# Kernel optimization log

Measured on AMD Instinct MI355X. Metric: run time of the kernel, lower is better.

Reference implementation:

```python
import jax, jax.numpy as jnp
import numpy as np

N, R, H0, H1, E, NB = 50000, 16, 128, 64, 800000, 8


def setup_inputs() -> dict:
    key = jax.random.key(0)
    k = jax.random.split(key, 6)
    nodes = jax.random.normal(k[0], (N, H0), dtype=jnp.float32)
    comps = jax.random.normal(k[1], (R, NB), dtype=jnp.float32) * 0.1
    bases = jax.random.normal(k[2], (NB, H0, H1), dtype=jnp.float32) * 0.05
    bias = jnp.zeros((H1,), dtype=jnp.float32)
    src = jax.random.randint(k[3], (E,), 0, N)
    rel = jax.random.randint(k[4], (E,), 0, R)
    dst = jax.random.randint(k[5], (E,), 0, N)
    return {"nodes": nodes, "comps": comps, "bases": bases, "bias": bias,
            "src": src, "rel": rel, "dst": dst}


def reference(nodes, comps, bases, bias, src, rel, dst):
    n, h0 = nodes.shape
    r = comps.shape[0]
    # Edge normalization: util.sum_sparse on the VERTICAL stacking -> row index
    # is rel*n + src, so each edge value is 1 / (#edges with same (rel, subject)).
    row = rel * n + src  # (E,)
    counts = jax.ops.segment_sum(jnp.ones(src.shape, jnp.float32), row, num_segments=r * n)
    vals = 1.0 / counts[row]  # (E,)
    # Basis decomposition: weights[r] = sum_b comps[r,b] * bases[b]
    weights = jnp.einsum('rb,bio->rio', comps, bases)  # (r, h0, h1)
    # Per-relation transformed node features (equivalent to expand + 'rni,rio->rno')
    nw = jnp.einsum('ni,rio->rno', nodes, weights)  # (r, n, h1)
    # Horizontal sparse mm: out[s] += val * nw[rel, dst]
    msgs = nw[rel, dst] * vals[:, None]  # (E, h1) gather
    out = jax.ops.segment_sum(msgs, src, num_segments=n)  # (n, h1) scatter-add
    return out + bias
```

## Files before the change

kernel.cpp:

```cpp
#include <hip/hip_runtime.h>
#include <hip/hip_bf16.h>

#define NN 50000
#define RR 16
#define H0 128
#define H1 64
#define EE 800000
#define NBASE 8
#define NTILES (NN / 16)
#define NGRPS ((NTILES + 3) / 4)
#define GEMM_BLOCKS NGRPS
#define COUNT_BLOCKS ((EE + 255) / 256)
#define NM (NN * RR)
#define NB1 782

typedef __attribute__((ext_vector_type(8))) short short8;
typedef __attribute__((ext_vector_type(4))) short short4v;
typedef __attribute__((ext_vector_type(4))) float f32x4;

__device__ inline short f2bs(float x) {
    __hip_bfloat16 b = __float2bfloat16(x);
    return *reinterpret_cast<short*>(&b);
}

__global__ void k_prep(const float* __restrict__ comps, const float* __restrict__ bases,
                       __hip_bfloat16* __restrict__ wtT, int* __restrict__ cnt) {
    if (blockIdx.x < 512) {
        int idx = blockIdx.x * 256 + threadIdx.x;
        int r = idx / (H1 * H0);
        int rem = idx % (H1 * H0);
        int o = rem / H0;
        int i = rem % H0;
        float acc = 0.0f;
#pragma unroll
        for (int b = 0; b < NBASE; ++b)
            acc += comps[r * NBASE + b] * bases[(b * H0 + i) * H1 + o];
        wtT[idx] = __float2bfloat16(acc);
    } else {
        int g = (blockIdx.x - 512) * 256 + threadIdx.x;
        if (g * 4 < NM) *(int4*)&cnt[g * 4] = (int4){0, 0, 0, 0};
    }
}

__global__ __launch_bounds__(256, 1)
void k_fused(const float* __restrict__ nodes,
             const __hip_bfloat16* __restrict__ wtT,
             __hip_bfloat16* __restrict__ nw,
             const int* __restrict__ src, const int* __restrict__ rel,
             int* __restrict__ cnt, int* __restrict__ rank) {
    __shared__ __hip_bfloat16 asmem[64 * 128];
    if (blockIdx.x < GEMM_BLOCKS) {
        int tid  = threadIdx.x;
        int ngrp = blockIdx.x;
        int ntl = NTILES - ngrp * 4;
        if (ntl > 4) ntl = 4;

#pragma unroll
        for (int i = 0; i < 8; ++i) {
            int f = i * 256 + tid;
            int row = f >> 5;
            int chunk = f & 31;
            int node = ngrp * 64 + row;
            if (node > NN - 1) node = NN - 1;
            float4 v = *(const float4*)&nodes[(size_t)node * H0 + chunk * 4];
            short4v o;
            o[0] = f2bs(v.x); o[1] = f2bs(v.y); o[2] = f2bs(v.z); o[3] = f2bs(v.w);
            int blk = chunk >> 1, half = chunk & 1;
            *(short4v*)((char*)asmem + row * 256 + ((blk ^ (row & 7)) << 4) + half * 8) = o;
        }
        __syncthreads();

        int wid  = tid >> 6;
        int lane = tid & 63;
        int rg   = wid;
        int n16  = lane & 15;
        int kg   = lane >> 4;

        short8 afrag[4][4];
#pragma unroll
        for (int t = 0; t < 4; ++t) {
            if (t < ntl) {
                int r = t * 16 + n16;
#pragma unroll
                for (int ks = 0; ks < 4; ++ks)
                    afrag[t][ks] = *(const short8*)((char*)asmem + r * 256 +
                                                    (((ks * 4 + kg) ^ (n16 & 7)) << 4));
            }
        }

        int chb = (n16 >> 2) * 16 + (n16 & 3);

        for (int r0 = 0; r0 < 4; ++r0) {
            int r = rg * 4 + r0;
            const __hip_bfloat16* wrr = &wtT[((size_t)r * H1 + chb) * H0 + kg * 8];
            f32x4 acc[4][4];
#pragma unroll
            for (int ot = 0; ot < 4; ++ot)
#pragma unroll
                for (int t = 0; t < 4; ++t) acc[ot][t] = (f32x4){0, 0, 0, 0};

#pragma unroll
            for (int ot = 0; ot < 4; ++ot) {
#pragma unroll
                for (int ks = 0; ks < 4; ++ks) {
                    short8 w = *(const short8*)(wrr + (size_t)(ot * 4) * H0 + ks * 32);
                    acc[ot][0] = __builtin_amdgcn_mfma_f32_16x16x32_bf16(w, afrag[0][ks], acc[ot][0], 0, 0, 0);
                    acc[ot][1] = __builtin_amdgcn_mfma_f32_16x16x32_bf16(w, afrag[1][ks], acc[ot][1], 0, 0, 0);
                    acc[ot][2] = __builtin_amdgcn_mfma_f32_16x16x32_bf16(w, afrag[2][ks], acc[ot][2], 0, 0, 0);
                    acc[ot][3] = __builtin_amdgcn_mfma_f32_16x16x32_bf16(w, afrag[3][ks], acc[ot][3], 0, 0, 0);
                }
            }

#pragma unroll
            for (int t = 0; t < 4; ++t) {
                if (t >= ntl) break;
                unsigned pk[8];
#pragma unroll
                for (int j = 0; j < 8; ++j) {
                    f32x4 a = acc[j >> 1][t];
                    float lo = a[(j & 1) * 2], hi = a[(j & 1) * 2 + 1];
                    pk[j] = (unsigned)(unsigned short)f2bs(lo) |
                            ((unsigned)(unsigned short)f2bs(hi) << 16);
                }
                uint4 q0; q0.x = pk[0]; q0.y = pk[1]; q0.z = pk[2]; q0.w = pk[3];
                uint4 q1; q1.x = pk[4]; q1.y = pk[5]; q1.z = pk[6]; q1.w = pk[7];
                char* rowp = (char*)nw +
                             ((size_t)r * NN + (size_t)ngrp * 64 + t * 16 + n16) * 128;
                *(uint4*)(rowp + kg * 16)      = q0;
                *(uint4*)(rowp + 64 + kg * 16) = q1;
            }
        }
    } else {
        int e = (blockIdx.x - GEMM_BLOCKS) * 256 + threadIdx.x;
        if (e < EE) {
            int bin = src[e] * RR + rel[e];
            rank[e] = atomicAdd(&cnt[bin], 1);
        }
    }
}

__global__ void k_scan1(const int* __restrict__ cnt, int* __restrict__ base2,
                        int* __restrict__ bsums) {
    __shared__ int tmp[256];
    int tid = threadIdx.x;
    int g = blockIdx.x * 256 + tid;
    int4 v = {0, 0, 0, 0};
    if (g * 4 < NM) v = *(const int4*)&cnt[g * 4];
    int s = v.x + v.y + v.z + v.w;
    tmp[tid] = s;
    __syncthreads();
    for (int off = 1; off < 256; off <<= 1) {
        int t = (tid >= off) ? tmp[tid - off] : 0;
        __syncthreads();
        tmp[tid] += t;
        __syncthreads();
    }
    int excl = tmp[tid] - s;
    if (tid == 255) bsums[blockIdx.x] = tmp[255];
    if (g * 4 < NM) {
        int4 o;
        o.x = excl;
        o.y = excl + v.x;
        o.z = excl + v.x + v.y;
        o.w = excl + v.x + v.y + v.z;
        *(int4*)&base2[g * 4] = o;
    }
}

__global__ void k_scan2(const int* __restrict__ bsums, int* __restrict__ bsofs) {
    __shared__ int tmp[256];
    int t = threadIdx.x;
    int i0 = t * 4;
    int v0 = (i0 < NB1) ? bsums[i0] : 0;
    int v1 = (i0 + 1 < NB1) ? bsums[i0 + 1] : 0;
    int v2 = (i0 + 2 < NB1) ? bsums[i0 + 2] : 0;
    int v3 = (i0 + 3 < NB1) ? bsums[i0 + 3] : 0;
    int tot = v0 + v1 + v2 + v3;
    tmp[t] = tot;
    __syncthreads();
    for (int off = 1; off < 256; off <<= 1) {
        int x = (t >= off) ? tmp[t - off] : 0;
        __syncthreads();
        tmp[t] += x;
        __syncthreads();
    }
    int excl = tmp[t] - tot;
    if (i0 < NB1)     bsofs[i0]     = excl;
    if (i0 + 1 < NB1) bsofs[i0 + 1] = excl + v0;
    if (i0 + 2 < NB1) bsofs[i0 + 2] = excl + v0 + v1;
    if (i0 + 3 < NB1) bsofs[i0 + 3] = excl + v0 + v1 + v2;
}

__global__ void k_place(const int* __restrict__ src, const int* __restrict__ rel,
                        const int* __restrict__ dst, const int* __restrict__ base2,
                        const int* __restrict__ bsofs, const int* __restrict__ rank,
                        unsigned* __restrict__ recs) {
    int e = blockIdx.x * blockDim.x + threadIdx.x;
    if (e < EE) {
        int bin = src[e] * RR + rel[e];
        int pos = base2[bin] + bsofs[bin >> 10] + rank[e];
        recs[pos] = ((unsigned)rel[e] << 16) | (unsigned)dst[e];
    }
}

__global__ void k_accum(const int* __restrict__ cnt, const int* __restrict__ base2,
                        const int* __restrict__ bsofs, const unsigned* __restrict__ recs,
                        const __hip_bfloat16* __restrict__ nw, const float* __restrict__ bias,
                        float* __restrict__ out) {
    __shared__ float inv[4][16];
    int w = threadIdx.x >> 6;
    int s = blockIdx.x * 4 + w;
    int lane = threadIdx.x & 63;
    if (s >= NN) return;
    if (lane < 16) inv[w][lane] = 1.0f / (float)cnt[s * RR + lane];
    int pl = ((lane >> 3) & 1) * 32 + (lane >> 4) * 8 + (lane & 7);
    int i0 = s * RR;
    int b0 = base2[i0] + bsofs[i0 >> 10];
    int b1 = (s == NN - 1) ? EE : base2[i0 + RR] + bsofs[(i0 + RR) >> 10];
    int n = b1 - b0;
    float a0 = bias[lane], a1 = 0.0f, a2 = 0.0f, a3 = 0.0f;
    int i = 0;
    for (; i + 4 <= n; i += 4) {
        unsigned rec0 = recs[b0 + i], rec1 = recs[b0 + i + 1];
        unsigned rec2 = recs[b0 + i + 2], rec3 = recs[b0 + i + 3];
        int r0 = rec0 >> 16, d0 = rec0 & 0xFFFF;
        int r1 = rec1 >> 16, d1 = rec1 & 0xFFFF;
        int r2 = rec2 >> 16, d2 = rec2 & 0xFFFF;
        int r3 = rec3 >> 16, d3 = rec3 & 0xFFFF;
        float m0 = __bfloat162float(nw[((size_t)r0 * NN + d0) * H1 + pl]);
        float m1 = __bfloat162float(nw[((size_t)r1 * NN + d1) * H1 + pl]);
        float m2 = __bfloat162float(nw[((size_t)r2 * NN + d2) * H1 + pl]);
        float m3 = __bfloat162float(nw[((size_t)r3 * NN + d3) * H1 + pl]);
        a0 += inv[w][r0] * m0;
        a1 += inv[w][r1] * m1;
        a2 += inv[w][r2] * m2;
        a3 += inv[w][r3] * m3;
    }
    for (; i < n; ++i) {
        unsigned rec = recs[b0 + i];
        int r = rec >> 16, d = rec & 0xFFFF;
        a0 += inv[w][r] * __bfloat162float(nw[((size_t)r * NN + d) * H1 + pl]);
    }
    out[(size_t)s * H1 + lane] = (a0 + a1) + (a2 + a3);
}

__global__ void k_init_out(float* __restrict__ out, const float* __restrict__ bias) {
    int i = blockIdx.x * blockDim.x + threadIdx.x;
    if (i < NN * H1) out[i] = bias[i & (H1 - 1)];
}

__global__ void k_count_only(const int* __restrict__ src, const int* __restrict__ rel,
                             float* __restrict__ counts) {
    int e = blockIdx.x * blockDim.x + threadIdx.x;
    if (e < EE) atomicAdd(&counts[rel[e] * NN + src[e]], 1.0f);
}

__global__ void k_weights_fb(const float* __restrict__ comps, const float* __restrict__ bases,
                             __hip_bfloat16* __restrict__ wtT) {
    int idx = blockIdx.x * blockDim.x + threadIdx.x;
    if (idx >= RR * H1 * H0) return;
    int r = idx / (H1 * H0);
    int rem = idx % (H1 * H0);
    int o = rem / H0;
    int i = rem % H0;
    float acc = 0.0f;
#pragma unroll
    for (int b = 0; b < NBASE; ++b)
        acc += comps[r * NBASE + b] * bases[(b * H0 + i) * H1 + o];
    wtT[idx] = __float2bfloat16(acc);
}

__global__ void k_fused_edge(const int* __restrict__ src, const int* __restrict__ rel,
                             const int* __restrict__ dst, const float* __restrict__ nodes,
                             const float* __restrict__ counts,
                             const __hip_bfloat16* __restrict__ wtT, float* __restrict__ out) {
    int e = blockIdx.x * (blockDim.x >> 6) + (threadIdx.x >> 6);
    int lane = threadIdx.x & 63;
    if (e >= EE) return;
    int s = src[e], r = rel[e], d = dst[e];
    float val = 1.0f / counts[r * NN + s];
    const __hip_bfloat16* w = &wtT[(size_t)(r * H1 + lane) * H0];
    const float* nd = &nodes[(size_t)d * H0];
    float acc = 0.0f;
#pragma unroll 8
    for (int i = 0; i < H0; ++i) acc += nd[i] * __bfloat162float(w[i]);
    atomicAdd(&out[s * H1 + lane], acc * val);
}

extern "C" void kernel_launch(void* const* d_in, const int* in_sizes, int n_in,
                              void* d_out, int out_size, void* d_ws, size_t ws_size,
                              hipStream_t stream) {
    const float* nodes = (const float*)d_in[0];
    const float* comps = (const float*)d_in[1];
    const float* bases = (const float*)d_in[2];
    const float* bias  = (const float*)d_in[3];
    const int*   src   = (const int*)d_in[4];
    const int*   rel   = (const int*)d_in[5];
    const int*   dst   = (const int*)d_in[6];
    float* out = (float*)d_out;

    char* ws = (char*)d_ws;
    int*   cnt           = (int*)ws;
    int*   base2         = (int*)(ws + 3200256);
    int*   bsums         = (int*)(ws + 6400512);
    int*   bsofs         = (int*)(ws + 6403968);
    __hip_bfloat16* wtT  = (__hip_bfloat16*)(ws + 6407424);
    int*   rank          = (int*)(ws + 6669824);
    unsigned* recs       = (unsigned*)(ws + 9870080);
    __hip_bfloat16* nw   = (__hip_bfloat16*)(ws + 13070080);
    const size_t need_full = 13070080ull + (size_t)RR * NN * H1 * 2ull;

    if (ws_size >= need_full) {
        k_prep<<<512 + 782, 256, 0, stream>>>(comps, bases, wtT, cnt);
        k_fused<<<GEMM_BLOCKS + COUNT_BLOCKS, 256, 0, stream>>>(nodes, wtT, nw, src, rel, cnt, rank);
        k_scan1<<<NB1, 256, 0, stream>>>(cnt, base2, bsums);
        k_scan2<<<1, 256, 0, stream>>>(bsums, bsofs);
        k_place<<<(EE + 255) / 256, 256, 0, stream>>>(src, rel, dst, base2, bsofs, rank, recs);
        k_accum<<<(NN + 3) / 4, 256, 0, stream>>>(cnt, base2, bsofs, recs, nw, bias, out);
    } else {
        float* countsF = (float*)ws;
        __hip_bfloat16* wtT2 = (__hip_bfloat16*)(ws + 3200256);
        (void)hipMemsetAsync(countsF, 0, (size_t)NM * 4, stream);
        k_count_only<<<(EE + 255) / 256, 256, 0, stream>>>(src, rel, countsF);
        k_weights_fb<<<(RR * H1 * H0 + 255) / 256, 256, 0, stream>>>(comps, bases, wtT2);
        k_init_out<<<(NN * H1 + 255) / 256, 256, 0, stream>>>(out, bias);
        k_fused_edge<<<EE / 4, 256, 0, stream>>>(src, rel, dst, nodes, countsF, wtT2, out);
    }
}
```

Baseline: 128.6 us.

## Merge scan passes with last-block ticket, vectorize count/place, widen accumulate unroll

Drops the separate second-level scan kernel: every scan1 block takes an atomic ticket after writing its block sum, and the last block to arrive scans the block sums. Counting and placement now handle four edges per thread with int4 loads, and the counting blocks are placed ahead of the GEMM blocks in the fused launch. The accumulation loop is unrolled by eight with independent accumulators to keep more gathers in flight. The aim is less launch overhead and more memory-level parallelism, at the cost of threadfence/atomic ordering logic and more registers in the accumulate kernel.

```diff
diff --git a/kernel.cpp b/kernel.cpp
--- a/kernel.cpp
+++ b/kernel.cpp
@@ -9,8 +9,8 @@
 #define NBASE 8
 #define NTILES (NN / 16)
 #define NGRPS ((NTILES + 3) / 4)
-#define GEMM_BLOCKS NGRPS
-#define COUNT_BLOCKS ((EE + 255) / 256)
+#define CB4 782
+#define PB4 782
 #define NM (NN * RR)
 #define NB1 782
 
@@ -24,7 +24,8 @@
 }
 
 __global__ void k_prep(const float* __restrict__ comps, const float* __restrict__ bases,
-                       __hip_bfloat16* __restrict__ wtT, int* __restrict__ cnt) {
+                       __hip_bfloat16* __restrict__ wtT, int* __restrict__ cnt,
+                       int* __restrict__ done) {
     if (blockIdx.x < 512) {
         int idx = blockIdx.x * 256 + threadIdx.x;
         int r = idx / (H1 * H0);
@@ -37,6 +38,7 @@
             acc += comps[r * NBASE + b] * bases[(b * H0 + i) * H1 + o];
         wtT[idx] = __float2bfloat16(acc);
     } else {
+        if (blockIdx.x == 512 && threadIdx.x == 0) done[0] = 0;
         int g = (blockIdx.x - 512) * 256 + threadIdx.x;
         if (g * 4 < NM) *(int4*)&cnt[g * 4] = (int4){0, 0, 0, 0};
     }
@@ -49,99 +51,113 @@
              const int* __restrict__ src, const int* __restrict__ rel,
              int* __restrict__ cnt, int* __restrict__ rank) {
     __shared__ __hip_bfloat16 asmem[64 * 128];
-    if (blockIdx.x < GEMM_BLOCKS) {
-        int tid  = threadIdx.x;
-        int ngrp = blockIdx.x;
-        int ntl = NTILES - ngrp * 4;
-        if (ntl > 4) ntl = 4;
-
-#pragma unroll
-        for (int i = 0; i < 8; ++i) {
-            int f = i * 256 + tid;
-            int row = f >> 5;
-            int chunk = f & 31;
-            int node = ngrp * 64 + row;
-            if (node > NN - 1) node = NN - 1;
-            float4 v = *(const float4*)&nodes[(size_t)node * H0 + chunk * 4];
-            short4v o;
-            o[0] = f2bs(v.x); o[1] = f2bs(v.y); o[2] = f2bs(v.z); o[3] = f2bs(v.w);
-            int blk = chunk >> 1, half = chunk & 1;
-            *(short4v*)((char*)asmem + row * 256 + ((blk ^ (row & 7)) << 4) + half * 8) = o;
-        }
-        __syncthreads();
-
-        int wid  = tid >> 6;
-        int lane = tid & 63;
-        int rg   = wid;
-        int n16  = lane & 15;
-        int kg   = lane >> 4;
-
-        short8 afrag[4][4];
+    if (blockIdx.x < CB4) {
+        int e0 = (blockIdx.x * 256 + (int)threadIdx.x) * 4;
+        if (e0 + 3 < EE) {
+            int4 s4 = *(const int4*)&src[e0];
+            int4 r4 = *(const int4*)&rel[e0];
+            int4 k;
+            k.x = atomicAdd(&cnt[s4.x * RR + r4.x], 1);
+            k.y = atomicAdd(&cnt[s4.y * RR + r4.y], 1);
+            k.z = atomicAdd(&cnt[s4.z * RR + r4.z], 1);
+            k.w = atomicAdd(&cnt[s4.w * RR + r4.w], 1);
+            *(int4*)&rank[e0] = k;
+        } else {
+            for (int j = 0; j < 4; ++j) {
+                int e = e0 + j;
+                if (e < EE) rank[e] = atomicAdd(&cnt[src[e] * RR + rel[e]], 1);
+            }
+        }
+        return;
+    }
+
+    int tid  = threadIdx.x;
+    int ngrp = blockIdx.x - CB4;
+    int ntl = NTILES - ngrp * 4;
+    if (ntl > 4) ntl = 4;
+
+#pragma unroll
+    for (int i = 0; i < 8; ++i) {
+        int f = i * 256 + tid;
+        int row = f >> 5;
+        int chunk = f & 31;
+        int node = ngrp * 64 + row;
+        if (node > NN - 1) node = NN - 1;
+        float4 v = *(const float4*)&nodes[(size_t)node * H0 + chunk * 4];
+        short4v o;
+        o[0] = f2bs(v.x); o[1] = f2bs(v.y); o[2] = f2bs(v.z); o[3] = f2bs(v.w);
+        int blk = chunk >> 1, half = chunk & 1;
+        *(short4v*)((char*)asmem + row * 256 + ((blk ^ (row & 7)) << 4) + half * 8) = o;
+    }
+    __syncthreads();
+
+    int wid  = tid >> 6;
+    int lane = tid & 63;
+    int rg   = wid;
+    int n16  = lane & 15;
+    int kg   = lane >> 4;
+
+    short8 afrag[4][4];
+#pragma unroll
+    for (int t = 0; t < 4; ++t) {
+        if (t < ntl) {
+            int r = t * 16 + n16;
+#pragma unroll
+            for (int ks = 0; ks < 4; ++ks)
+                afrag[t][ks] = *(const short8*)((char*)asmem + r * 256 +
+                                                (((ks * 4 + kg) ^ (n16 & 7)) << 4));
+        }
+    }
+
+    int chb = (n16 >> 2) * 16 + (n16 & 3);
+
+    for (int r0 = 0; r0 < 4; ++r0) {
+        int r = rg * 4 + r0;
+        const __hip_bfloat16* wrr = &wtT[((size_t)r * H1 + chb) * H0 + kg * 8];
+        f32x4 acc[4][4];
+#pragma unroll
+        for (int ot = 0; ot < 4; ++ot)
+#pragma unroll
+            for (int t = 0; t < 4; ++t) acc[ot][t] = (f32x4){0, 0, 0, 0};
+
+#pragma unroll
+        for (int ot = 0; ot < 4; ++ot) {
+#pragma unroll
+            for (int ks = 0; ks < 4; ++ks) {
+                short8 w = *(const short8*)(wrr + (size_t)(ot * 4) * H0 + ks * 32);
+                acc[ot][0] = __builtin_amdgcn_mfma_f32_16x16x32_bf16(w, afrag[0][ks], acc[ot][0], 0, 0, 0);
+                acc[ot][1] = __builtin_amdgcn_mfma_f32_16x16x32_bf16(w, afrag[1][ks], acc[ot][1], 0, 0, 0);
+                acc[ot][2] = __builtin_amdgcn_mfma_f32_16x16x32_bf16(w, afrag[2][ks], acc[ot][2], 0, 0, 0);
+                acc[ot][3] = __builtin_amdgcn_mfma_f32_16x16x32_bf16(w, afrag[3][ks], acc[ot][3], 0, 0, 0);
+            }
+        }
+
 #pragma unroll
         for (int t = 0; t < 4; ++t) {
-            if (t < ntl) {
-                int r = t * 16 + n16;
-#pragma unroll
-                for (int ks = 0; ks < 4; ++ks)
-                    afrag[t][ks] = *(const short8*)((char*)asmem + r * 256 +
-                                                    (((ks * 4 + kg) ^ (n16 & 7)) << 4));
+            if (t >= ntl) break;
+            unsigned pk[8];
+#pragma unroll
+            for (int j = 0; j < 8; ++j) {
+                f32x4 a = acc[j >> 1][t];
+                float lo = a[(j & 1) * 2], hi = a[(j & 1) * 2 + 1];
+                pk[j] = (unsigned)(unsigned short)f2bs(lo) |
+                        ((unsigned)(unsigned short)f2bs(hi) << 16);
             }
-        }
-
-        int chb = (n16 >> 2) * 16 + (n16 & 3);
-
-        for (int r0 = 0; r0 < 4; ++r0) {
-            int r = rg * 4 + r0;
-            const __hip_bfloat16* wrr = &wtT[((size_t)r * H1 + chb) * H0 + kg * 8];
-            f32x4 acc[4][4];
-#pragma unroll
-            for (int ot = 0; ot < 4; ++ot)
-#pragma unroll
-                for (int t = 0; t < 4; ++t) acc[ot][t] = (f32x4){0, 0, 0, 0};
-
-#pragma unroll
-            for (int ot = 0; ot < 4; ++ot) {
-#pragma unroll
-                for (int ks = 0; ks < 4; ++ks) {
-                    short8 w = *(const short8*)(wrr + (size_t)(ot * 4) * H0 + ks * 32);
-                    acc[ot][0] = __builtin_amdgcn_mfma_f32_16x16x32_bf16(w, afrag[0][ks], acc[ot][0], 0, 0, 0);
-                    acc[ot][1] = __builtin_amdgcn_mfma_f32_16x16x32_bf16(w, afrag[1][ks], acc[ot][1], 0, 0, 0);
-                    acc[ot][2] = __builtin_amdgcn_mfma_f32_16x16x32_bf16(w, afrag[2][ks], acc[ot][2], 0, 0, 0);
-                    acc[ot][3] = __builtin_amdgcn_mfma_f32_16x16x32_bf16(w, afrag[3][ks], acc[ot][3], 0, 0, 0);
-                }
-            }
-
-#pragma unroll
-            for (int t = 0; t < 4; ++t) {
-                if (t >= ntl) break;
-                unsigned pk[8];
-#pragma unroll
-                for (int j = 0; j < 8; ++j) {
-                    f32x4 a = acc[j >> 1][t];
-                    float lo = a[(j & 1) * 2], hi = a[(j & 1) * 2 + 1];
-                    pk[j] = (unsigned)(unsigned short)f2bs(lo) |
-                            ((unsigned)(unsigned short)f2bs(hi) << 16);
-                }
-                uint4 q0; q0.x = pk[0]; q0.y = pk[1]; q0.z = pk[2]; q0.w = pk[3];
-                uint4 q1; q1.x = pk[4]; q1.y = pk[5]; q1.z = pk[6]; q1.w = pk[7];
-                char* rowp = (char*)nw +
-                             ((size_t)r * NN + (size_t)ngrp * 64 + t * 16 + n16) * 128;
-                *(uint4*)(rowp + kg * 16)      = q0;
-                *(uint4*)(rowp + 64 + kg * 16) = q1;
-            }
-        }
-    } else {
-        int e = (blockIdx.x - GEMM_BLOCKS) * 256 + threadIdx.x;
-        if (e < EE) {
-            int bin = src[e] * RR + rel[e];
-            rank[e] = atomicAdd(&cnt[bin], 1);
+            uint4 q0; q0.x = pk[0]; q0.y = pk[1]; q0.z = pk[2]; q0.w = pk[3];
+            uint4 q1; q1.x = pk[4]; q1.y = pk[5]; q1.z = pk[6]; q1.w = pk[7];
+            char* rowp = (char*)nw +
+                         ((size_t)r * NN + (size_t)ngrp * 64 + t * 16 + n16) * 128;
+            *(uint4*)(rowp + kg * 16)      = q0;
+            *(uint4*)(rowp + 64 + kg * 16) = q1;
         }
     }
 }
 
 __global__ void k_scan1(const int* __restrict__ cnt, int* __restrict__ base2,
-                        int* __restrict__ bsums) {
+                        int* __restrict__ bsums, int* __restrict__ bsofs,
+                        int* __restrict__ done) {
     __shared__ int tmp[256];
+    __shared__ int ticket;
     int tid = threadIdx.x;
     int g = blockIdx.x * 256 + tid;
     int4 v = {0, 0, 0, 0};
@@ -165,41 +181,58 @@
         o.w = excl + v.x + v.y + v.z;
         *(int4*)&base2[g * 4] = o;
     }
-}
-
-__global__ void k_scan2(const int* __restrict__ bsums, int* __restrict__ bsofs) {
-    __shared__ int tmp[256];
-    int t = threadIdx.x;
-    int i0 = t * 4;
+    __threadfence();
+    if (tid == 0) ticket = atomicAdd(done, 1);
+    __syncthreads();
+    if (ticket != NB1 - 1) return;
+    __threadfence();
+    int i0 = tid * 4;
     int v0 = (i0 < NB1) ? bsums[i0] : 0;
     int v1 = (i0 + 1 < NB1) ? bsums[i0 + 1] : 0;
     int v2 = (i0 + 2 < NB1) ? bsums[i0 + 2] : 0;
     int v3 = (i0 + 3 < NB1) ? bsums[i0 + 3] : 0;
     int tot = v0 + v1 + v2 + v3;
-    tmp[t] = tot;
+    __syncthreads();
+    tmp[tid] = tot;
     __syncthreads();
     for (int off = 1; off < 256; off <<= 1) {
-        int x = (t >= off) ? tmp[t - off] : 0;
+        int x = (tid >= off) ? tmp[tid - off] : 0;
         __syncthreads();
-        tmp[t] += x;
+        tmp[tid] += x;
         __syncthreads();
     }
-    int excl = tmp[t] - tot;
-    if (i0 < NB1)     bsofs[i0]     = excl;
-    if (i0 + 1 < NB1) bsofs[i0 + 1] = excl + v0;
-    if (i0 + 2 < NB1) bsofs[i0 + 2] = excl + v0 + v1;
-    if (i0 + 3 < NB1) bsofs[i0 + 3] = excl + v0 + v1 + v2;
+    int excl2 = tmp[tid] - tot;
+    if (i0 < NB1)     bsofs[i0]     = excl2;
+    if (i0 + 1 < NB1) bsofs[i0 + 1] = excl2 + v0;
+    if (i0 + 2 < NB1) bsofs[i0 + 2] = excl2 + v0 + v1;
+    if (i0 + 3 < NB1) bsofs[i0 + 3] = excl2 + v0 + v1 + v2;
 }
 
 __global__ void k_place(const int* __restrict__ src, const int* __restrict__ rel,
                         const int* __restrict__ dst, const int* __restrict__ base2,
                         const int* __restrict__ bsofs, const int* __restrict__ rank,
                         unsigned* __restrict__ recs) {
-    int e = blockIdx.x * blockDim.x + threadIdx.x;
-    if (e < EE) {
-        int bin = src[e] * RR + rel[e];
-        int pos = base2[bin] + bsofs[bin >> 10] + rank[e];
-        recs[pos] = ((unsigned)rel[e] << 16) | (unsigned)dst[e];
+    int e0 = (blockIdx.x * 256 + (int)threadIdx.x) * 4;
+    if (e0 + 3 < EE) {
+        int4 s4 = *(const int4*)&src[e0];
+        int4 r4 = *(const int4*)&rel[e0];
+        int4 d4 = *(const int4*)&dst[e0];
+        int4 k4 = *(const int4*)&rank[e0];
+        int b0 = s4.x * RR + r4.x, b1 = s4.y * RR + r4.y;
+        int b2 = s4.z * RR + r4.z, b3 = s4.w * RR + r4.w;
+        recs[base2[b0] + bsofs[b0 >> 10] + k4.x] = ((unsigned)r4.x << 16) | (unsigned)d4.x;
+        recs[base2[b1] + bsofs[b1 >> 10] + k4.y] = ((unsigned)r4.y << 16) | (unsigned)d4.y;
+        recs[base2[b2] + bsofs[b2 >> 10] + k4.z] = ((unsigned)r4.z << 16) | (unsigned)d4.z;
+        recs[base2[b3] + bsofs[b3 >> 10] + k4.w] = ((unsigned)r4.w << 16) | (unsigned)d4.w;
+    } else {
+        for (int j = 0; j < 4; ++j) {
+            int e = e0 + j;
+            if (e < EE) {
+                int bin = src[e] * RR + rel[e];
+                recs[base2[bin] + bsofs[bin >> 10] + rank[e]] =
+                    ((unsigned)rel[e] << 16) | (unsigned)dst[e];
+            }
+        }
     }
 }
 
@@ -218,30 +251,39 @@
     int b0 = base2[i0] + bsofs[i0 >> 10];
     int b1 = (s == NN - 1) ? EE : base2[i0 + RR] + bsofs[(i0 + RR) >> 10];
     int n = b1 - b0;
-    float a0 = bias[lane], a1 = 0.0f, a2 = 0.0f, a3 = 0.0f;
+    float a[8];
+    a[0] = bias[lane];
+#pragma unroll
+    for (int j = 1; j < 8; ++j) a[j] = 0.0f;
     int i = 0;
-    for (; i + 4 <= n; i += 4) {
+    for (; i + 8 <= n; i += 8) {
+        unsigned rc[8]; int rr[8], dd[8]; float mm[8];
+#pragma unroll
+        for (int j = 0; j < 8; ++j) rc[j] = recs[b0 + i + j];
+#pragma unroll
+        for (int j = 0; j < 8; ++j) { rr[j] = rc[j] >> 16; dd[j] = rc[j] & 0xFFFF; }
+#pragma unroll
+        for (int j = 0; j < 8; ++j)
+            mm[j] = __bfloat162float(nw[((size_t)rr[j] * NN + dd[j]) * H1 + pl]);
+#pragma unroll
+        for (int j = 0; j < 8; ++j) a[j] += inv[w][rr[j]] * mm[j];
+    }
+    for (; i + 2 <= n; i += 2) {
         unsigned rec0 = recs[b0 + i], rec1 = recs[b0 + i + 1];
-        unsigned rec2 = recs[b0 + i + 2], rec3 = recs[b0 + i + 3];
         int r0 = rec0 >> 16, d0 = rec0 & 0xFFFF;
         int r1 = rec1 >> 16, d1 = rec1 & 0xFFFF;
-        int r2 = rec2 >> 16, d2 = rec2 & 0xFFFF;
-        int r3 = rec3 >> 16, d3 = rec3 & 0xFFFF;
         float m0 = __bfloat162float(nw[((size_t)r0 * NN + d0) * H1 + pl]);
         float m1 = __bfloat162float(nw[((size_t)r1 * NN + d1) * H1 + pl]);
-        float m2 = __bfloat162float(nw[((size_t)r2 * NN + d2) * H1 + pl]);
-        float m3 = __bfloat162float(nw[((size_t)r3 * NN + d3) * H1 + pl]);
-        a0 += inv[w][r0] * m0;
-        a1 += inv[w][r1] * m1;
-        a2 += inv[w][r2] * m2;
-        a3 += inv[w][r3] * m3;
-    }
-    for (; i < n; ++i) {
+        a[0] += inv[w][r0] * m0;
+        a[1] += inv[w][r1] * m1;
+    }
+    if (i < n) {
         unsigned rec = recs[b0 + i];
         int r = rec >> 16, d = rec & 0xFFFF;
-        a0 += inv[w][r] * __bfloat162float(nw[((size_t)r * NN + d) * H1 + pl]);
-    }
-    out[(size_t)s * H1 + lane] = (a0 + a1) + (a2 + a3);
+        a[0] += inv[w][r] * __bfloat162float(nw[((size_t)r * NN + d) * H1 + pl]);
+    }
+    out[(size_t)s * H1 + lane] = ((a[0] + a[1]) + (a[2] + a[3])) +
+                                 ((a[4] + a[5]) + (a[6] + a[7]));
 }
 
 __global__ void k_init_out(float* __restrict__ out, const float* __restrict__ bias) {
@@ -304,6 +346,7 @@
     int*   base2         = (int*)(ws + 3200256);
     int*   bsums         = (int*)(ws + 6400512);
     int*   bsofs         = (int*)(ws + 6403968);
+    int*   done          = (int*)(ws + 6407168);
     __hip_bfloat16* wtT  = (__hip_bfloat16*)(ws + 6407424);
     int*   rank          = (int*)(ws + 6669824);
     unsigned* recs       = (unsigned*)(ws + 9870080);
@@ -311,11 +354,10 @@
     const size_t need_full = 13070080ull + (size_t)RR * NN * H1 * 2ull;
 
     if (ws_size >= need_full) {
-        k_prep<<<512 + 782, 256, 0, stream>>>(comps, bases, wtT, cnt);
-        k_fused<<<GEMM_BLOCKS + COUNT_BLOCKS, 256, 0, stream>>>(nodes, wtT, nw, src, rel, cnt, rank);
-        k_scan1<<<NB1, 256, 0, stream>>>(cnt, base2, bsums);
-        k_scan2<<<1, 256, 0, stream>>>(bsums, bsofs);
-        k_place<<<(EE + 255) / 256, 256, 0, stream>>>(src, rel, dst, base2, bsofs, rank, recs);
+        k_prep<<<512 + 782, 256, 0, stream>>>(comps, bases, wtT, cnt, done);
+        k_fused<<<CB4 + NGRPS, 256, 0, stream>>>(nodes, wtT, nw, src, rel, cnt, rank);
+        k_scan1<<<NB1, 256, 0, stream>>>(cnt, base2, bsums, bsofs, done);
+        k_place<<<PB4, 256, 0, stream>>>(src, rel, dst, base2, bsofs, rank, recs);
         k_accum<<<(NN + 3) / 4, 256, 0, stream>>>(cnt, base2, bsofs, recs, nw, bias, out);
     } else {
         float* countsF = (float*)ws;
```

Result: slower. 202.2 us (+57.2%).

## Bucket edges by source only and compute relation counts per node in LDS

Applied to the files above, without the earlier changes.

Edge bucketing now keys on the source node instead of the (source, relation) pair. This shrinks the count array and both scan passes from 800k bins to 50k bins, and the count and place kernels no longer read rel to build the key. Per-relation edge counts, needed for the 1/count normalization, are rebuilt inside the accumulate kernel with a shared-memory histogram over each node's records. The price is an extra pass over each node's records plus LDS atomics and block-wide barriers in the accumulate kernel, and records within a node are no longer grouped by relation.

```diff
diff --git a/kernel.cpp b/kernel.cpp
--- a/kernel.cpp
+++ b/kernel.cpp
@@ -11,8 +11,7 @@
 #define NGRPS ((NTILES + 3) / 4)
 #define GEMM_BLOCKS NGRPS
 #define COUNT_BLOCKS ((EE + 255) / 256)
-#define NM (NN * RR)
-#define NB1 782
+#define NBS1 49
 
 typedef __attribute__((ext_vector_type(8))) short short8;
 typedef __attribute__((ext_vector_type(4))) short short4v;
@@ -24,7 +23,7 @@
 }
 
 __global__ void k_prep(const float* __restrict__ comps, const float* __restrict__ bases,
-                       __hip_bfloat16* __restrict__ wtT, int* __restrict__ cnt) {
+                       __hip_bfloat16* __restrict__ wtT, int* __restrict__ tot) {
     if (blockIdx.x < 512) {
         int idx = blockIdx.x * 256 + threadIdx.x;
         int r = idx / (H1 * H0);
@@ -38,7 +37,7 @@
         wtT[idx] = __float2bfloat16(acc);
     } else {
         int g = (blockIdx.x - 512) * 256 + threadIdx.x;
-        if (g * 4 < NM) *(int4*)&cnt[g * 4] = (int4){0, 0, 0, 0};
+        if (g * 4 < NN) *(int4*)&tot[g * 4] = (int4){0, 0, 0, 0};
     }
 }
 
@@ -46,8 +45,8 @@
 void k_fused(const float* __restrict__ nodes,
              const __hip_bfloat16* __restrict__ wtT,
              __hip_bfloat16* __restrict__ nw,
-             const int* __restrict__ src, const int* __restrict__ rel,
-             int* __restrict__ cnt, int* __restrict__ rank) {
+             const int* __restrict__ src,
+             int* __restrict__ tot, int* __restrict__ rank) {
     __shared__ __hip_bfloat16 asmem[64 * 128];
     if (blockIdx.x < GEMM_BLOCKS) {
         int tid  = threadIdx.x;
@@ -132,20 +131,17 @@
         }
     } else {
         int e = (blockIdx.x - GEMM_BLOCKS) * 256 + threadIdx.x;
-        if (e < EE) {
-            int bin = src[e] * RR + rel[e];
-            rank[e] = atomicAdd(&cnt[bin], 1);
-        }
-    }
-}
-
-__global__ void k_scan1(const int* __restrict__ cnt, int* __restrict__ base2,
+        if (e < EE) rank[e] = atomicAdd(&tot[src[e]], 1);
+    }
+}
+
+__global__ void k_scan1(const int* __restrict__ tot, int* __restrict__ base2,
                         int* __restrict__ bsums) {
     __shared__ int tmp[256];
     int tid = threadIdx.x;
     int g = blockIdx.x * 256 + tid;
     int4 v = {0, 0, 0, 0};
-    if (g * 4 < NM) v = *(const int4*)&cnt[g * 4];
+    if (g * 4 < NN) v = *(const int4*)&tot[g * 4];
     int s = v.x + v.y + v.z + v.w;
     tmp[tid] = s;
     __syncthreads();
@@ -157,7 +153,7 @@
     }
     int excl = tmp[tid] - s;
     if (tid == 255) bsums[blockIdx.x] = tmp[255];
-    if (g * 4 < NM) {
+    if (g * 4 < NN) {
         int4 o;
         o.x = excl;
         o.y = excl + v.x;
@@ -168,27 +164,18 @@
 }
 
 __global__ void k_scan2(const int* __restrict__ bsums, int* __restrict__ bsofs) {
-    __shared__ int tmp[256];
+    __shared__ int tmp[64];
     int t = threadIdx.x;
-    int i0 = t * 4;
-    int v0 = (i0 < NB1) ? bsums[i0] : 0;
-    int v1 = (i0 + 1 < NB1) ? bsums[i0 + 1] : 0;
-    int v2 = (i0 + 2 < NB1) ? bsums[i0 + 2] : 0;
-    int v3 = (i0 + 3 < NB1) ? bsums[i0 + 3] : 0;
-    int tot = v0 + v1 + v2 + v3;
-    tmp[t] = tot;
-    __syncthreads();
-    for (int off = 1; off < 256; off <<= 1) {
+    int v = (t < NBS1) ? bsums[t] : 0;
+    tmp[t] = v;
+    __syncthreads();
+    for (int off = 1; off < 64; off <<= 1) {
         int x = (t >= off) ? tmp[t - off] : 0;
         __syncthreads();
         tmp[t] += x;
         __syncthreads();
     }
-    int excl = tmp[t] - tot;
-    if (i0 < NB1)     bsofs[i0]     = excl;
-    if (i0 + 1 < NB1) bsofs[i0 + 1] = excl + v0;
-    if (i0 + 2 < NB1) bsofs[i0 + 2] = excl + v0 + v1;
-    if (i0 + 3 < NB1) bsofs[i0 + 3] = excl + v0 + v1 + v2;
+    if (t < NBS1) bsofs[t] = tmp[t] - v;
 }
 
 __global__ void k_place(const int* __restrict__ src, const int* __restrict__ rel,
@@ -197,27 +184,33 @@
                         unsigned* __restrict__ recs) {
     int e = blockIdx.x * blockDim.x + threadIdx.x;
     if (e < EE) {
-        int bin = src[e] * RR + rel[e];
-        int pos = base2[bin] + bsofs[bin >> 10] + rank[e];
+        int s = src[e];
+        int pos = base2[s] + bsofs[s >> 10] + rank[e];
         recs[pos] = ((unsigned)rel[e] << 16) | (unsigned)dst[e];
     }
 }
 
-__global__ void k_accum(const int* __restrict__ cnt, const int* __restrict__ base2,
-                        const int* __restrict__ bsofs, const unsigned* __restrict__ recs,
+__global__ void k_accum(const int* __restrict__ base2, const int* __restrict__ bsofs,
+                        const unsigned* __restrict__ recs,
                         const __hip_bfloat16* __restrict__ nw, const float* __restrict__ bias,
                         float* __restrict__ out) {
+    __shared__ int   hist[4][16];
     __shared__ float inv[4][16];
     int w = threadIdx.x >> 6;
     int s = blockIdx.x * 4 + w;
     int lane = threadIdx.x & 63;
-    if (s >= NN) return;
-    if (lane < 16) inv[w][lane] = 1.0f / (float)cnt[s * RR + lane];
+    int b0 = base2[s] + bsofs[s >> 10];
+    int b1 = (s == NN - 1) ? EE : base2[s + 1] + bsofs[(s + 1) >> 10];
+    int n = b1 - b0;
+    if (lane < 16) hist[w][lane] = 0;
+    __syncthreads();
+    for (int i = lane; i < n; i += 64)
+        atomicAdd(&hist[w][recs[b0 + i] >> 16], 1);
+    __syncthreads();
+    if (lane < 16) inv[w][lane] = 1.0f / (float)hist[w][lane];
+    __syncthreads();
+
     int pl = ((lane >> 3) & 1) * 32 + (lane >> 4) * 8 + (lane & 7);
-    int i0 = s * RR;
-    int b0 = base2[i0] + bsofs[i0 >> 10];
-    int b1 = (s == NN - 1) ? EE : base2[i0 + RR] + bsofs[(i0 + RR) >> 10];
-    int n = b1 - b0;
     float a0 = bias[lane], a1 = 0.0f, a2 = 0.0f, a3 = 0.0f;
     int i = 0;
     for (; i + 4 <= n; i += 4) {
@@ -300,7 +293,7 @@
     float* out = (float*)d_out;
 
     char* ws = (char*)d_ws;
-    int*   cnt           = (int*)ws;
+    int*   tot           = (int*)ws;
     int*   base2         = (int*)(ws + 3200256);
     int*   bsums         = (int*)(ws + 6400512);
     int*   bsofs         = (int*)(ws + 6403968);
@@ -311,16 +304,16 @@
     const size_t need_full = 13070080ull + (size_t)RR * NN * H1 * 2ull;
 
     if (ws_size >= need_full) {
-        k_prep<<<512 + 782, 256, 0, stream>>>(comps, bases, wtT, cnt);
-        k_fused<<<GEMM_BLOCKS + COUNT_BLOCKS, 256, 0, stream>>>(nodes, wtT, nw, src, rel, cnt, rank);
-        k_scan1<<<NB1, 256, 0, stream>>>(cnt, base2, bsums);
-        k_scan2<<<1, 256, 0, stream>>>(bsums, bsofs);
+        k_prep<<<512 + NBS1, 256, 0, stream>>>(comps, bases, wtT, tot);
+        k_fused<<<GEMM_BLOCKS + COUNT_BLOCKS, 256, 0, stream>>>(nodes, wtT, nw, src, tot, rank);
+        k_scan1<<<NBS1, 256, 0, stream>>>(tot, base2, bsums);
+        k_scan2<<<1, 64, 0, stream>>>(bsums, bsofs);
         k_place<<<(EE + 255) / 256, 256, 0, stream>>>(src, rel, dst, base2, bsofs, rank, recs);
-        k_accum<<<(NN + 3) / 4, 256, 0, stream>>>(cnt, base2, bsofs, recs, nw, bias, out);
+        k_accum<<<NN / 4, 256, 0, stream>>>(base2, bsofs, recs, nw, bias, out);
     } else {
         float* countsF = (float*)ws;
         __hip_bfloat16* wtT2 = (__hip_bfloat16*)(ws + 3200256);
-        (void)hipMemsetAsync(countsF, 0, (size_t)NM * 4, stream);
+        (void)hipMemsetAsync(countsF, 0, (size_t)NN * RR * 4, stream);
         k_count_only<<<(EE + 255) / 256, 256, 0, stream>>>(src, rel, countsF);
         k_weights_fb<<<(RR * H1 * H0 + 255) / 256, 256, 0, stream>>>(comps, bases, wtT2);
         k_init_out<<<(NN * H1 + 255) / 256, 256, 0, stream>>>(out, bias);
```

Measured after the change: 125.1 us. 2.7% less time.
